# Performance work log

Hardware: AMD Instinct MI355X
Metric: run time of the kernel (lower is better)

The kernel has to match this reference:

```python
import jax, jax.numpy as jnp
import numpy as np

B, S, D, H = 4, 2048, 512, 8
DK = D // H
SCALE = 1.0 / np.sqrt(DK)


def setup_inputs() -> dict:
    key = jax.random.key(0)
    kx, kq, kk, kv = jax.random.split(key, 4)
    w_std = np.sqrt(2.0 / (D + D))  # xavier-ish scale
    return {
        "x": jax.random.normal(kx, (B, S, D), dtype=jnp.float32),
        "W_Q": jax.random.normal(kq, (D, D), dtype=jnp.float32) * w_std,
        "W_K": jax.random.normal(kk, (D, D), dtype=jnp.float32) * w_std,
        "W_V": jax.random.normal(kv, (D, D), dtype=jnp.float32) * w_std,
    }


def reference(x, W_Q, W_K, W_V):
    # torch Linear(bias=False): y = x @ W.T
    q = jnp.einsum('bsd,ed->bse', x, W_Q).reshape(B, S, H, DK).transpose(0, 2, 1, 3)
    k = jnp.einsum('bsd,ed->bse', x, W_K).reshape(B, S, H, DK).transpose(0, 2, 1, 3)
    v = jnp.einsum('bsd,ed->bse', x, W_V).reshape(B, S, H, DK).transpose(0, 2, 1, 3)
    scores = jnp.einsum('bhqd,bhkd->bhqk', q, k) * SCALE  # [B,H,S,S]
    scores_exp = jnp.exp(scores)  # faithful: no max-subtraction in original
    attn = scores_exp / (scores_exp.sum(axis=-1, keepdims=True) + 1e-8)
    context = jnp.einsum('bhqk,bhkd->bhqd', attn, v)
    return context.transpose(0, 2, 1, 3).reshape(B, S, D)
```

## Files before the change

kernel.cpp:

```cpp
#include <hip/hip_runtime.h>
#include <hip/hip_bf16.h>

#define Bsz 4
#define Ssz 2048
#define Dsz 512
#define Hsz 8
#define DKsz 64

typedef __bf16 bf16x8 __attribute__((ext_vector_type(8)));
typedef __bf16 bf16x4 __attribute__((ext_vector_type(4)));
typedef float f32x4 __attribute__((ext_vector_type(4)));

#define SWE(c, row) ((((c) ^ ((row) & 7)) * 8))

__global__ __launch_bounds__(256) void cvt_kernel(
    const float* __restrict__ x, const float* __restrict__ Wq,
    const float* __restrict__ Wk, const float* __restrict__ Wv,
    __bf16* __restrict__ xb, __bf16* __restrict__ Wb)
{
    const int i = blockIdx.x * 256 + threadIdx.x;
    const int XN4 = (Bsz * Ssz * Dsz) / 4;
    const float* src;
    __bf16* dst;
    int off;
    if (i < XN4) {
        src = x; dst = xb; off = i;
    } else {
        int j = i - XN4;
        int w = j >> 16;
        off = j & 65535;
        src = (w == 0) ? Wq : (w == 1) ? Wk : Wv;
        dst = Wb + (size_t)w * (Dsz * Dsz);
    }
    float4 v = ((const float4*)src)[off];
    __bf16 o[4] = {(__bf16)v.x, (__bf16)v.y, (__bf16)v.z, (__bf16)v.w};
    *(uint2*)(dst + (size_t)off * 4) = *(uint2*)o;
}

template<bool VM>
__device__ __forceinline__ void qkv_body(
    const __bf16* __restrict__ xb, const __bf16* __restrict__ W,
    __bf16* __restrict__ dst, float scale)
{
    __shared__ __bf16 xs[128][64];
    __shared__ __bf16 wsh[128][64];

    const int tid  = threadIdx.x;
    const int lane = tid & 63;
    const int wave = tid >> 6;
    const int quad = lane >> 4;
    const int l16  = lane & 15;
    const int wm   = (wave & 1) * 64;
    const int wn   = (wave >> 1) * 64;

    const int tm = blockIdx.x * 128;
    const int tn = blockIdx.y * 128;

    const int srow = tid >> 1;
    const int c0   = (tid & 1) * 4;

    const __bf16* xg = xb + (size_t)(tm + srow) * Dsz;
    const __bf16* wg = W  + (size_t)(tn + srow) * Dsz;

    bf16x8 px[4], pw[4];
    #pragma unroll
    for (int i = 0; i < 4; ++i) {
        px[i] = *(const bf16x8*)(xg + (c0 + i) * 8);
        pw[i] = *(const bf16x8*)(wg + (c0 + i) * 8);
    }

    f32x4 acc[4][4];
    #pragma unroll
    for (int i = 0; i < 4; ++i)
        #pragma unroll
        for (int j = 0; j < 4; ++j) acc[i][j] = (f32x4){0.f, 0.f, 0.f, 0.f};

    for (int k0 = 0; k0 < Dsz; k0 += 64) {
        __syncthreads();
        #pragma unroll
        for (int i = 0; i < 4; ++i) {
            *(bf16x8*)&xs[srow][SWE(c0 + i, srow)]  = px[i];
            *(bf16x8*)&wsh[srow][SWE(c0 + i, srow)] = pw[i];
        }
        __syncthreads();
        if (k0 + 64 < Dsz) {
            #pragma unroll
            for (int i = 0; i < 4; ++i) {
                px[i] = *(const bf16x8*)(xg + k0 + 64 + (c0 + i) * 8);
                pw[i] = *(const bf16x8*)(wg + k0 + 64 + (c0 + i) * 8);
            }
        }

        #pragma unroll
        for (int kk = 0; kk < 2; ++kk) {
            bf16x8 fa[4], fb[4];
            #pragma unroll
            for (int mi = 0; mi < 4; ++mi) {
                const int row = wm + mi * 16 + l16;
                fa[mi] = VM ? *(const bf16x8*)&xs[row][SWE(kk * 4 + quad, row)]
                            : *(const bf16x8*)&wsh[row][SWE(kk * 4 + quad, row)];
            }
            #pragma unroll
            for (int ni = 0; ni < 4; ++ni) {
                const int row = wn + ni * 16 + l16;
                fb[ni] = VM ? *(const bf16x8*)&wsh[row][SWE(kk * 4 + quad, row)]
                            : *(const bf16x8*)&xs[row][SWE(kk * 4 + quad, row)];
            }
            #pragma unroll
            for (int mi = 0; mi < 4; ++mi)
                #pragma unroll
                for (int ni = 0; ni < 4; ++ni)
                    acc[mi][ni] = __builtin_amdgcn_mfma_f32_16x16x32_bf16(
                        fa[mi], fb[ni], acc[mi][ni], 0, 0, 0);
        }
    }

    if (!VM) {
        #pragma unroll
        for (int mi = 0; mi < 4; ++mi) {
            const int e0 = tn + wm + mi * 16 + quad * 4;
            const int h = e0 >> 6, d0 = e0 & 63;
            #pragma unroll
            for (int ni = 0; ni < 4; ++ni) {
                const int sf = tm + wn + ni * 16 + l16;
                const int b = sf >> 11, s = sf & (Ssz - 1);
                bf16x4 p;
                #pragma unroll
                for (int r = 0; r < 4; ++r) p[r] = (__bf16)(acc[mi][ni][r] * scale);
                *(bf16x4*)&dst[((((size_t)(b * Hsz + h) * Ssz + s)) << 6) + d0] = p;
            }
        }
    } else {
        #pragma unroll
        for (int mi = 0; mi < 4; ++mi) {
            const int sf0 = tm + wm + mi * 16 + quad * 4;
            const int b = sf0 >> 11, s0 = sf0 & (Ssz - 1);
            #pragma unroll
            for (int ni = 0; ni < 4; ++ni) {
                const int e = tn + wn + ni * 16 + l16;
                const int h = e >> 6, d = e & 63;
                bf16x4 p;
                #pragma unroll
                for (int r = 0; r < 4; ++r) p[r] = (__bf16)acc[mi][ni][r];
                *(bf16x4*)&dst[(((size_t)(b * Hsz + h) * DKsz + d) << 11) + s0] = p;
            }
        }
    }
}

__global__ __launch_bounds__(256, 2) void qkv_qk_kernel(
    const __bf16* __restrict__ xb, const __bf16* __restrict__ Wb,
    __bf16* __restrict__ Qo, __bf16* __restrict__ Ko)
{
    const int which = blockIdx.z;
    const float qscale = 0.125f * 1.44269504088896340736f;
    qkv_body<false>(xb, Wb + (size_t)which * (Dsz * Dsz),
                    which == 0 ? Qo : Ko, which == 0 ? qscale : 1.0f);
}

__global__ __launch_bounds__(256, 2) void qkv_v_kernel(
    const __bf16* __restrict__ xb, const __bf16* __restrict__ Wb,
    __bf16* __restrict__ Vo)
{
    qkv_body<true>(xb, Wb + (size_t)2 * (Dsz * Dsz), Vo, 1.0f);
}

__global__ __launch_bounds__(256, 1) void attn_kernel(
    const __bf16* __restrict__ Q, const __bf16* __restrict__ K,
    const __bf16* __restrict__ VT, float* __restrict__ out)
{
    __shared__ __bf16 ks[64][64];
    __shared__ __bf16 vs[64][64];
    __shared__ __bf16 ps[4][16][64];

    const int tid  = threadIdx.x;
    const int lane = tid & 63;
    const int wave = tid >> 6;
    const int quad = lane >> 4;
    const int l16  = lane & 15;

    const int bh = blockIdx.x;
    const int qt = blockIdx.y;
    const int b  = bh >> 3;
    const int h  = bh & 7;

    const __bf16* Qb = Q  + (size_t)bh * Ssz * DKsz;
    const __bf16* Kb = K  + (size_t)bh * Ssz * DKsz;
    const __bf16* Vb = VT + (size_t)bh * DKsz * Ssz;

    bf16x8 qf[4][2];
    #pragma unroll
    for (int qs = 0; qs < 4; ++qs) {
        const __bf16* qrow = Qb + (size_t)(qt * 256 + wave * 64 + qs * 16 + l16) * DKsz;
        qf[qs][0] = *(const bf16x8*)(qrow + quad * 8);
        qf[qs][1] = *(const bf16x8*)(qrow + 32 + quad * 8);
    }

    bf16x8 ones;
    #pragma unroll
    for (int i = 0; i < 8; ++i) ones[i] = (__bf16)1.0f;

    f32x4 oacc[4][4];
    #pragma unroll
    for (int qs = 0; qs < 4; ++qs)
        #pragma unroll
        for (int i = 0; i < 4; ++i) oacc[qs][i] = (f32x4){0.f, 0.f, 0.f, 0.f};
    f32x4 lacc[4];
    #pragma unroll
    for (int qs = 0; qs < 4; ++qs) lacc[qs] = (f32x4){0.f, 0.f, 0.f, 0.f};

    const int srow = tid >> 2;
    const int c0   = tid & 3;

    bf16x8 pk0 = *(const bf16x8*)(Kb + (size_t)srow * DKsz + c0 * 8);
    bf16x8 pk1 = *(const bf16x8*)(Kb + (size_t)srow * DKsz + (c0 + 4) * 8);
    bf16x8 pv0 = *(const bf16x8*)(Vb + (size_t)srow * Ssz + c0 * 8);
    bf16x8 pv1 = *(const bf16x8*)(Vb + (size_t)srow * Ssz + (c0 + 4) * 8);

    for (int kb = 0; kb < Ssz; kb += 64) {
        __syncthreads();
        *(bf16x8*)&ks[srow][SWE(c0, srow)]     = pk0;
        *(bf16x8*)&ks[srow][SWE(c0 + 4, srow)] = pk1;
        *(bf16x8*)&vs[srow][SWE(c0, srow)]     = pv0;
        *(bf16x8*)&vs[srow][SWE(c0 + 4, srow)] = pv1;
        __syncthreads();

        if (kb + 64 < Ssz) {
            pk0 = *(const bf16x8*)(Kb + (size_t)(kb + 64 + srow) * DKsz + c0 * 8);
            pk1 = *(const bf16x8*)(Kb + (size_t)(kb + 64 + srow) * DKsz + (c0 + 4) * 8);
            pv0 = *(const bf16x8*)(Vb + (size_t)srow * Ssz + kb + 64 + c0 * 8);
            pv1 = *(const bf16x8*)(Vb + (size_t)srow * Ssz + kb + 64 + (c0 + 4) * 8);
        }

        bf16x8 kf[2][4], vf[2][4];
        #pragma unroll
        for (int kk = 0; kk < 2; ++kk)
            #pragma unroll
            for (int ns = 0; ns < 4; ++ns) {
                const int row = ns * 16 + l16;
                kf[kk][ns] = *(const bf16x8*)&ks[row][SWE(kk * 4 + quad, row)];
                vf[kk][ns] = *(const bf16x8*)&vs[row][SWE(kk * 4 + quad, row)];
            }

        #pragma unroll
        for (int qs = 0; qs < 4; ++qs) {
            f32x4 sacc[4];
            #pragma unroll
            for (int ns = 0; ns < 4; ++ns) {
                sacc[ns] = (f32x4){0.f, 0.f, 0.f, 0.f};
                sacc[ns] = __builtin_amdgcn_mfma_f32_16x16x32_bf16(qf[qs][0], kf[0][ns], sacc[ns], 0, 0, 0);
                sacc[ns] = __builtin_amdgcn_mfma_f32_16x16x32_bf16(qf[qs][1], kf[1][ns], sacc[ns], 0, 0, 0);
            }
            #pragma unroll
            for (int ns = 0; ns < 4; ++ns) {
                const int c = ns * 2 + (l16 >> 3);
                #pragma unroll
                for (int r = 0; r < 4; ++r) {
                    const int prow = quad * 4 + r;
                    ps[wave][prow][SWE(c, prow) + (l16 & 7)] =
                        (__bf16)__builtin_amdgcn_exp2f(sacc[ns][r]);
                }
            }
            bf16x8 af0 = *(const bf16x8*)&ps[wave][l16][SWE(quad, l16)];
            bf16x8 af1 = *(const bf16x8*)&ps[wave][l16][SWE(4 + quad, l16)];
            #pragma unroll
            for (int ns = 0; ns < 4; ++ns) {
                oacc[qs][ns] = __builtin_amdgcn_mfma_f32_16x16x32_bf16(vf[0][ns], af0, oacc[qs][ns], 0, 0, 0);
                oacc[qs][ns] = __builtin_amdgcn_mfma_f32_16x16x32_bf16(vf[1][ns], af1, oacc[qs][ns], 0, 0, 0);
            }
            lacc[qs] = __builtin_amdgcn_mfma_f32_16x16x32_bf16(ones, af0, lacc[qs], 0, 0, 0);
            lacc[qs] = __builtin_amdgcn_mfma_f32_16x16x32_bf16(ones, af1, lacc[qs], 0, 0, 0);
        }
    }

    #pragma unroll
    for (int qs = 0; qs < 4; ++qs) {
        const float linv = 1.f / (lacc[qs][0] + 1e-8f);
        const int q = qt * 256 + wave * 64 + qs * 16 + l16;
        float* obase = out + ((size_t)b * Ssz + q) * Dsz + h * DKsz;
        #pragma unroll
        for (int ns = 0; ns < 4; ++ns) {
            f32x4 o = oacc[qs][ns] * linv;
            *(f32x4*)(obase + ns * 16 + quad * 4) = o;
        }
    }
}

extern "C" void kernel_launch(void* const* d_in, const int* in_sizes, int n_in,
                              void* d_out, int out_size, void* d_ws, size_t ws_size,
                              hipStream_t stream) {
    const float* x  = (const float*)d_in[0];
    const float* Wq = (const float*)d_in[1];
    const float* Wk = (const float*)d_in[2];
    const float* Wv = (const float*)d_in[3];
    float* out = (float*)d_out;

    const size_t per = (size_t)Bsz * Hsz * Ssz * DKsz;
    __bf16* Qw  = (__bf16*)d_ws;
    __bf16* Kw  = Qw + per;
    __bf16* VTw = Kw + per;
    __bf16* xb  = VTw + per;
    __bf16* Wb  = xb + per;

    cvt_kernel<<<4864, 256, 0, stream>>>(x, Wq, Wk, Wv, xb, Wb);
    qkv_qk_kernel<<<dim3((Bsz * Ssz) / 128, Dsz / 128, 2), 256, 0, stream>>>(xb, Wb, Qw, Kw);
    qkv_v_kernel<<<dim3((Bsz * Ssz) / 128, Dsz / 128), 256, 0, stream>>>(xb, Wb, VTw);
    attn_kernel<<<dim3(Bsz * Hsz, Ssz / 256), 256, 0, stream>>>(Qw, Kw, VTw, out);
}
```

Before: 162.7 us.

## Merge QKV projection kernels and load attention K/V fragments directly to registers

The three projection GEMMs now run in one launch with blockIdx.z selecting Q, K or V, and the shared-memory operand roles are swapped at runtime instead of by template. The attention kernel drops its shared-memory K/V tiles and barriers. Each wave loads its K and V MFMA fragments straight from global memory into registers, double-buffered one 64-key tile ahead. The query tile is halved to 128 rows per block, doubling the grid, with occupancy raised to 2 blocks per CU. This removes LDS staging and __syncthreads in the inner loop, at the cost of each wave redundantly fetching K/V from global/L2 and holding more registers.

Measured after the change: 213.2 us. 1.31x slower.

```diff
diff --git a/kernel.cpp b/kernel.cpp
--- a/kernel.cpp
+++ b/kernel.cpp
@@ -37,10 +37,9 @@
     *(uint2*)(dst + (size_t)off * 4) = *(uint2*)o;
 }
 
-template<bool VM>
-__device__ __forceinline__ void qkv_body(
-    const __bf16* __restrict__ xb, const __bf16* __restrict__ W,
-    __bf16* __restrict__ dst, float scale)
+__global__ __launch_bounds__(256, 3) void qkv_kernel(
+    const __bf16* __restrict__ xb, const __bf16* __restrict__ Wb,
+    __bf16* __restrict__ Qo, __bf16* __restrict__ Ko, __bf16* __restrict__ Vo)
 {
     __shared__ __bf16 xs[128][64];
     __shared__ __bf16 wsh[128][64];
@@ -55,6 +54,9 @@
 
     const int tm = blockIdx.x * 128;
     const int tn = blockIdx.y * 128;
+    const int which = blockIdx.z;
+    const bool VM = (which == 2);
+    const __bf16* W = Wb + (size_t)which * (Dsz * Dsz);
 
     const int srow = tid >> 1;
     const int c0   = (tid & 1) * 4;
@@ -75,6 +77,9 @@
         #pragma unroll
         for (int j = 0; j < 4; ++j) acc[i][j] = (f32x4){0.f, 0.f, 0.f, 0.f};
 
+    const __bf16 (*Ash)[64] = VM ? xs : wsh;
+    const __bf16 (*Bsh)[64] = VM ? wsh : xs;
+
     for (int k0 = 0; k0 < Dsz; k0 += 64) {
         __syncthreads();
         #pragma unroll
@@ -97,14 +102,12 @@
             #pragma unroll
             for (int mi = 0; mi < 4; ++mi) {
                 const int row = wm + mi * 16 + l16;
-                fa[mi] = VM ? *(const bf16x8*)&xs[row][SWE(kk * 4 + quad, row)]
-                            : *(const bf16x8*)&wsh[row][SWE(kk * 4 + quad, row)];
+                fa[mi] = *(const bf16x8*)&Ash[row][SWE(kk * 4 + quad, row)];
             }
             #pragma unroll
             for (int ni = 0; ni < 4; ++ni) {
                 const int row = wn + ni * 16 + l16;
-                fb[ni] = VM ? *(const bf16x8*)&wsh[row][SWE(kk * 4 + quad, row)]
-                            : *(const bf16x8*)&xs[row][SWE(kk * 4 + quad, row)];
+                fb[ni] = *(const bf16x8*)&Bsh[row][SWE(kk * 4 + quad, row)];
             }
             #pragma unroll
             for (int mi = 0; mi < 4; ++mi)
@@ -116,6 +119,8 @@
     }
 
     if (!VM) {
+        const float scale = (which == 0) ? 0.125f * 1.44269504088896340736f : 1.0f;
+        __bf16* dst = (which == 0) ? Qo : Ko;
         #pragma unroll
         for (int mi = 0; mi < 4; ++mi) {
             const int e0 = tn + wm + mi * 16 + quad * 4;
@@ -142,36 +147,17 @@
                 bf16x4 p;
                 #pragma unroll
                 for (int r = 0; r < 4; ++r) p[r] = (__bf16)acc[mi][ni][r];
-                *(bf16x4*)&dst[(((size_t)(b * Hsz + h) * DKsz + d) << 11) + s0] = p;
-            }
-        }
-    }
-}
-
-__global__ __launch_bounds__(256, 2) void qkv_qk_kernel(
-    const __bf16* __restrict__ xb, const __bf16* __restrict__ Wb,
-    __bf16* __restrict__ Qo, __bf16* __restrict__ Ko)
-{
-    const int which = blockIdx.z;
-    const float qscale = 0.125f * 1.44269504088896340736f;
-    qkv_body<false>(xb, Wb + (size_t)which * (Dsz * Dsz),
-                    which == 0 ? Qo : Ko, which == 0 ? qscale : 1.0f);
-}
-
-__global__ __launch_bounds__(256, 2) void qkv_v_kernel(
-    const __bf16* __restrict__ xb, const __bf16* __restrict__ Wb,
-    __bf16* __restrict__ Vo)
-{
-    qkv_body<true>(xb, Wb + (size_t)2 * (Dsz * Dsz), Vo, 1.0f);
-}
-
-__global__ __launch_bounds__(256, 1) void attn_kernel(
+                *(bf16x4*)&Vo[(((size_t)(b * Hsz + h) * DKsz + d) << 11) + s0] = p;
+            }
+        }
+    }
+}
+
+__global__ __launch_bounds__(256, 2) void attn_kernel(
     const __bf16* __restrict__ Q, const __bf16* __restrict__ K,
     const __bf16* __restrict__ VT, float* __restrict__ out)
 {
-    __shared__ __bf16 ks[64][64];
-    __shared__ __bf16 vs[64][64];
-    __shared__ __bf16 ps[4][16][64];
+    __shared__ __bf16 ps[4][2][16][64];
 
     const int tid  = threadIdx.x;
     const int lane = tid & 63;
@@ -188,10 +174,10 @@
     const __bf16* Kb = K  + (size_t)bh * Ssz * DKsz;
     const __bf16* Vb = VT + (size_t)bh * DKsz * Ssz;
 
-    bf16x8 qf[4][2];
-    #pragma unroll
-    for (int qs = 0; qs < 4; ++qs) {
-        const __bf16* qrow = Qb + (size_t)(qt * 256 + wave * 64 + qs * 16 + l16) * DKsz;
+    bf16x8 qf[2][2];
+    #pragma unroll
+    for (int qs = 0; qs < 2; ++qs) {
+        const __bf16* qrow = Qb + (size_t)(qt * 128 + wave * 32 + qs * 16 + l16) * DKsz;
         qf[qs][0] = *(const bf16x8*)(qrow + quad * 8);
         qf[qs][1] = *(const bf16x8*)(qrow + 32 + quad * 8);
     }
@@ -200,56 +186,42 @@
     #pragma unroll
     for (int i = 0; i < 8; ++i) ones[i] = (__bf16)1.0f;
 
-    f32x4 oacc[4][4];
-    #pragma unroll
-    for (int qs = 0; qs < 4; ++qs)
+    f32x4 oacc[2][4];
+    #pragma unroll
+    for (int qs = 0; qs < 2; ++qs)
         #pragma unroll
         for (int i = 0; i < 4; ++i) oacc[qs][i] = (f32x4){0.f, 0.f, 0.f, 0.f};
-    f32x4 lacc[4];
-    #pragma unroll
-    for (int qs = 0; qs < 4; ++qs) lacc[qs] = (f32x4){0.f, 0.f, 0.f, 0.f};
-
-    const int srow = tid >> 2;
-    const int c0   = tid & 3;
-
-    bf16x8 pk0 = *(const bf16x8*)(Kb + (size_t)srow * DKsz + c0 * 8);
-    bf16x8 pk1 = *(const bf16x8*)(Kb + (size_t)srow * DKsz + (c0 + 4) * 8);
-    bf16x8 pv0 = *(const bf16x8*)(Vb + (size_t)srow * Ssz + c0 * 8);
-    bf16x8 pv1 = *(const bf16x8*)(Vb + (size_t)srow * Ssz + (c0 + 4) * 8);
-
+    f32x4 lacc[2] = {(f32x4){0.f, 0.f, 0.f, 0.f}, (f32x4){0.f, 0.f, 0.f, 0.f}};
+
+    bf16x8 kc[2][4], vc[2][4], kn[2][4], vn[2][4];
+    #pragma unroll
+    for (int kk = 0; kk < 2; ++kk)
+        #pragma unroll
+        for (int ns = 0; ns < 4; ++ns) {
+            kc[kk][ns] = *(const bf16x8*)(Kb + (size_t)(ns * 16 + l16) * DKsz + kk * 32 + quad * 8);
+            vc[kk][ns] = *(const bf16x8*)(Vb + (size_t)(ns * 16 + l16) * Ssz + kk * 32 + quad * 8);
+        }
+
+    #pragma unroll 2
     for (int kb = 0; kb < Ssz; kb += 64) {
-        __syncthreads();
-        *(bf16x8*)&ks[srow][SWE(c0, srow)]     = pk0;
-        *(bf16x8*)&ks[srow][SWE(c0 + 4, srow)] = pk1;
-        *(bf16x8*)&vs[srow][SWE(c0, srow)]     = pv0;
-        *(bf16x8*)&vs[srow][SWE(c0 + 4, srow)] = pv1;
-        __syncthreads();
-
         if (kb + 64 < Ssz) {
-            pk0 = *(const bf16x8*)(Kb + (size_t)(kb + 64 + srow) * DKsz + c0 * 8);
-            pk1 = *(const bf16x8*)(Kb + (size_t)(kb + 64 + srow) * DKsz + (c0 + 4) * 8);
-            pv0 = *(const bf16x8*)(Vb + (size_t)srow * Ssz + kb + 64 + c0 * 8);
-            pv1 = *(const bf16x8*)(Vb + (size_t)srow * Ssz + kb + 64 + (c0 + 4) * 8);
-        }
-
-        bf16x8 kf[2][4], vf[2][4];
-        #pragma unroll
-        for (int kk = 0; kk < 2; ++kk)
-            #pragma unroll
-            for (int ns = 0; ns < 4; ++ns) {
-                const int row = ns * 16 + l16;
-                kf[kk][ns] = *(const bf16x8*)&ks[row][SWE(kk * 4 + quad, row)];
-                vf[kk][ns] = *(const bf16x8*)&vs[row][SWE(kk * 4 + quad, row)];
-            }
-
-        #pragma unroll
-        for (int qs = 0; qs < 4; ++qs) {
+            #pragma unroll
+            for (int kk = 0; kk < 2; ++kk)
+                #pragma unroll
+                for (int ns = 0; ns < 4; ++ns) {
+                    kn[kk][ns] = *(const bf16x8*)(Kb + (size_t)(kb + 64 + ns * 16 + l16) * DKsz + kk * 32 + quad * 8);
+                    vn[kk][ns] = *(const bf16x8*)(Vb + (size_t)(ns * 16 + l16) * Ssz + kb + 64 + kk * 32 + quad * 8);
+                }
+        }
+
+        #pragma unroll
+        for (int qs = 0; qs < 2; ++qs) {
             f32x4 sacc[4];
             #pragma unroll
             for (int ns = 0; ns < 4; ++ns) {
                 sacc[ns] = (f32x4){0.f, 0.f, 0.f, 0.f};
-                sacc[ns] = __builtin_amdgcn_mfma_f32_16x16x32_bf16(qf[qs][0], kf[0][ns], sacc[ns], 0, 0, 0);
-                sacc[ns] = __builtin_amdgcn_mfma_f32_16x16x32_bf16(qf[qs][1], kf[1][ns], sacc[ns], 0, 0, 0);
+                sacc[ns] = __builtin_amdgcn_mfma_f32_16x16x32_bf16(qf[qs][0], kc[0][ns], sacc[ns], 0, 0, 0);
+                sacc[ns] = __builtin_amdgcn_mfma_f32_16x16x32_bf16(qf[qs][1], kc[1][ns], sacc[ns], 0, 0, 0);
             }
             #pragma unroll
             for (int ns = 0; ns < 4; ++ns) {
@@ -257,26 +229,34 @@
                 #pragma unroll
                 for (int r = 0; r < 4; ++r) {
                     const int prow = quad * 4 + r;
-                    ps[wave][prow][SWE(c, prow) + (l16 & 7)] =
+                    ps[wave][qs][prow][SWE(c, prow) + (l16 & 7)] =
                         (__bf16)__builtin_amdgcn_exp2f(sacc[ns][r]);
                 }
             }
-            bf16x8 af0 = *(const bf16x8*)&ps[wave][l16][SWE(quad, l16)];
-            bf16x8 af1 = *(const bf16x8*)&ps[wave][l16][SWE(4 + quad, l16)];
-            #pragma unroll
-            for (int ns = 0; ns < 4; ++ns) {
-                oacc[qs][ns] = __builtin_amdgcn_mfma_f32_16x16x32_bf16(vf[0][ns], af0, oacc[qs][ns], 0, 0, 0);
-                oacc[qs][ns] = __builtin_amdgcn_mfma_f32_16x16x32_bf16(vf[1][ns], af1, oacc[qs][ns], 0, 0, 0);
+            bf16x8 af0 = *(const bf16x8*)&ps[wave][qs][l16][SWE(quad, l16)];
+            bf16x8 af1 = *(const bf16x8*)&ps[wave][qs][l16][SWE(4 + quad, l16)];
+            #pragma unroll
+            for (int ns = 0; ns < 4; ++ns) {
+                oacc[qs][ns] = __builtin_amdgcn_mfma_f32_16x16x32_bf16(vc[0][ns], af0, oacc[qs][ns], 0, 0, 0);
+                oacc[qs][ns] = __builtin_amdgcn_mfma_f32_16x16x32_bf16(vc[1][ns], af1, oacc[qs][ns], 0, 0, 0);
             }
             lacc[qs] = __builtin_amdgcn_mfma_f32_16x16x32_bf16(ones, af0, lacc[qs], 0, 0, 0);
             lacc[qs] = __builtin_amdgcn_mfma_f32_16x16x32_bf16(ones, af1, lacc[qs], 0, 0, 0);
         }
-    }
-
-    #pragma unroll
-    for (int qs = 0; qs < 4; ++qs) {
+
+        #pragma unroll
+        for (int kk = 0; kk < 2; ++kk)
+            #pragma unroll
+            for (int ns = 0; ns < 4; ++ns) {
+                kc[kk][ns] = kn[kk][ns];
+                vc[kk][ns] = vn[kk][ns];
+            }
+    }
+
+    #pragma unroll
+    for (int qs = 0; qs < 2; ++qs) {
         const float linv = 1.f / (lacc[qs][0] + 1e-8f);
-        const int q = qt * 256 + wave * 64 + qs * 16 + l16;
+        const int q = qt * 128 + wave * 32 + qs * 16 + l16;
         float* obase = out + ((size_t)b * Ssz + q) * Dsz + h * DKsz;
         #pragma unroll
         for (int ns = 0; ns < 4; ++ns) {
@@ -303,7 +283,7 @@
     __bf16* Wb  = xb + per;
 
     cvt_kernel<<<4864, 256, 0, stream>>>(x, Wq, Wk, Wv, xb, Wb);
-    qkv_qk_kernel<<<dim3((Bsz * Ssz) / 128, Dsz / 128, 2), 256, 0, stream>>>(xb, Wb, Qw, Kw);
-    qkv_v_kernel<<<dim3((Bsz * Ssz) / 128, Dsz / 128), 256, 0, stream>>>(xb, Wb, VTw);
-    attn_kernel<<<dim3(Bsz * Hsz, Ssz / 256), 256, 0, stream>>>(Qw, Kw, VTw, out);
-}
+    qkv_kernel<<<dim3((Bsz * Ssz) / 128, Dsz / 128, 3), 256, 0, stream>>>(
+        xb, Wb, Qw, Kw, VTw);
+    attn_kernel<<<dim3(Bsz * Hsz, Ssz / 128), 256, 0, stream>>>(Qw, Kw, VTw, out);
+}
```
